# Kernel tuning notes

Hardware: AMD Instinct MI355X
Metric: run time of the kernel (lower is better)

The kernel has to match this reference:

```python
import jax, jax.numpy as jnp
import numpy as np


def setup_inputs() -> dict:
    key = jax.random.key(0)
    ks = jax.random.split(key, 9)
    B, Cin, H, W = 16, 512, 64, 64
    Cout = 256
    s_in = 0.02  # small init scale for stable softmax
    return {
        "x": jax.random.normal(ks[0], (B, Cin, H, W), dtype=jnp.float32),
        "Wq": jax.random.normal(ks[1], (Cout, Cin), dtype=jnp.float32) * s_in,
        "bq": jnp.zeros((Cout,), dtype=jnp.float32),
        "Wk": jax.random.normal(ks[2], (Cout, Cin), dtype=jnp.float32) * s_in,
        "bk": jnp.zeros((Cout,), dtype=jnp.float32),
        "Wv": jax.random.normal(ks[3], (Cout, Cin), dtype=jnp.float32) * s_in,
        "bv": jnp.zeros((Cout,), dtype=jnp.float32),
        "Wo": jax.random.normal(ks[4], (Cin, Cout), dtype=jnp.float32) * s_in,
        "bo": jnp.zeros((Cin,), dtype=jnp.float32),
    }


def reference(x, Wq, bq, Wk, bk, Wv, bv, Wo, bo):
    B, C, H, W = x.shape
    N = H * W
    xf = x.reshape(B, C, N)  # flatten spatial
    # 1x1 convs == per-pixel linear maps over channels
    q = jnp.einsum('oc,bcn->bon', Wq, xf) + bq[None, :, None]  # [B,Cout,N]
    k = jnp.einsum('oc,bcn->bon', Wk, xf) + bk[None, :, None]
    v = jnp.einsum('oc,bcn->bon', Wv, xf) + bv[None, :, None]
    # NOTE: original contracts over spatial dim N -> channel-attention [B,Cout,Cout]
    scale = jnp.asarray(N, x.dtype) ** 0.5  # query.size(-1) == N
    scores = jnp.einsum('bcn,bdn->bcd', q, k) / scale
    attn = jax.nn.softmax(scores, axis=-1)  # softmax over key-channel dim
    out = jnp.einsum('bcd,bdn->bcn', attn, v)  # [B,Cout,N]
    # permute(0,2,1).view(B,-1,H,W): row-major reshape of (B,N,Cout)
    out = jnp.transpose(out, (0, 2, 1)).reshape(B, -1, H, W)  # [B,Cout,H,W]
    out = jnp.einsum('co,bohw->bchw', Wo, out) + bo[None, :, None, None]
    return out
```

## Files before the change

kernel.cpp:

```cpp
#include <hip/hip_runtime.h>
#include <math.h>

typedef unsigned short u16;
typedef __bf16 bf16x8 __attribute__((ext_vector_type(8)));
typedef float f32x4 __attribute__((ext_vector_type(4)));
typedef unsigned short u16x4 __attribute__((ext_vector_type(4)));
typedef unsigned short u16x8 __attribute__((ext_vector_type(8)));

__device__ __forceinline__ u16 f2bf(float f) {
    unsigned int u = __float_as_uint(f);
    return (u16)((u + 0x7FFF + ((u >> 16) & 1)) >> 16);
}

#define BAR() do { __builtin_amdgcn_sched_barrier(0); __builtin_amdgcn_s_barrier(); __builtin_amdgcn_sched_barrier(0); } while (0)

__device__ __forceinline__ void stage_half(
    const u16* __restrict__ g, int ld, int row0, int rstride, int kt,
    u16* lds, int w, int l)
{
    #pragma unroll
    for (int qq = 0; qq < 2; ++qq) {
        const int c0 = qq * 512 + w * 64;
        const int c  = c0 + l;
        const int r  = c >> 3, kc = c & 7;
        const int kcg = kc ^ (r & 7);
        const u16* src = g + (size_t)(row0 + r * rstride) * ld + kt + kcg * 8;
        __builtin_amdgcn_global_load_lds(
            (const __attribute__((address_space(1))) unsigned int*)src,
            (__attribute__((address_space(3))) unsigned int*)(lds + (size_t)c0 * 8),
            16, 0, 0);
    }
}

#define QUAD(q_) do {                                                          \
    bf16x8 af0[2], af1[2];                                                     \
    { int row = wm + ((q_) * 2 + 0) * 16 + p;                                  \
      af0[0] = *(const bf16x8*)(bufA + row * 64 + ((0 + g) ^ (row & 7)) * 8);  \
      af0[1] = *(const bf16x8*)(bufA + row * 64 + ((4 + g) ^ (row & 7)) * 8); }\
    { int row = wm + ((q_) * 2 + 1) * 16 + p;                                  \
      af1[0] = *(const bf16x8*)(bufA + row * 64 + ((0 + g) ^ (row & 7)) * 8);  \
      af1[1] = *(const bf16x8*)(bufA + row * 64 + ((4 + g) ^ (row & 7)) * 8); }\
    __builtin_amdgcn_s_setprio(1);                                             \
    _Pragma("unroll")                                                          \
    for (int nf = 0; nf < 4; ++nf) {                                           \
        acc[(q_)*2+0][nf] = __builtin_amdgcn_mfma_f32_16x16x32_bf16(af0[0], bfr[nf][0], acc[(q_)*2+0][nf], 0, 0, 0); \
        acc[(q_)*2+0][nf] = __builtin_amdgcn_mfma_f32_16x16x32_bf16(af0[1], bfr[nf][1], acc[(q_)*2+0][nf], 0, 0, 0); \
        acc[(q_)*2+1][nf] = __builtin_amdgcn_mfma_f32_16x16x32_bf16(af1[0], bfr[nf][0], acc[(q_)*2+1][nf], 0, 0, 0); \
        acc[(q_)*2+1][nf] = __builtin_amdgcn_mfma_f32_16x16x32_bf16(af1[1], bfr[nf][1], acc[(q_)*2+1][nf], 0, 0, 0); \
    }                                                                          \
    __builtin_amdgcn_s_setprio(0);                                             \
} while (0)

template<int NT>
__device__ __forceinline__ void gemm256(
    const u16* __restrict__ Ag, int ldA, int baseA, int rsA,
    const u16* __restrict__ Bg, int ldB, int n0,
    u16* sm, f32x4 (&acc)[8][4])
{
    const int tid = threadIdx.x;
    const int l = tid & 63, w = tid >> 6;
    const int p = l & 15, g = l >> 4;
    const int wm = (w >> 2) * 128;
    const int wn = (w & 3) * 64;

    stage_half(Ag, ldA, baseA,             rsA, 0, sm,         w, l);
    stage_half(Ag, ldA, baseA + 128 * rsA, rsA, 0, sm + 8192,  w, l);
    stage_half(Bg, ldB, n0,       1, 0, sm + 16384, w, l);
    stage_half(Bg, ldB, n0 + 128, 1, 0, sm + 24576, w, l);

    for (int t = 0; t < NT; ++t) {
        u16* bufA  = sm + (t & 1) * 32768;
        u16* bufB  = bufA + 16384;
        u16* nbufA = sm + ((t + 1) & 1) * 32768;
        u16* nbufB = nbufA + 16384;
        const int kt1 = (t + 1) * 64;

        if (t + 1 < NT) {
            stage_half(Ag, ldA, baseA,             rsA, kt1, nbufA,        w, l);
            stage_half(Ag, ldA, baseA + 128 * rsA, rsA, kt1, nbufA + 8192, w, l);
            asm volatile("s_waitcnt vmcnt(4)" ::: "memory");
        } else {
            asm volatile("s_waitcnt vmcnt(0)" ::: "memory");
        }
        BAR();
        bf16x8 bfr[4][2];
        #pragma unroll
        for (int nf = 0; nf < 4; ++nf) {
            int row = wn + nf * 16 + p;
            bfr[nf][0] = *(const bf16x8*)(bufB + row * 64 + ((0 + g) ^ (row & 7)) * 8);
            bfr[nf][1] = *(const bf16x8*)(bufB + row * 64 + ((4 + g) ^ (row & 7)) * 8);
        }
        QUAD(0);
        BAR();
        if (t + 1 < NT) stage_half(Bg, ldB, n0, 1, kt1, nbufB, w, l);
        QUAD(1);
        BAR();
        if (t + 1 < NT) stage_half(Bg, ldB, n0 + 128, 1, kt1, nbufB + 8192, w, l);
        QUAD(2);
        BAR();
        QUAD(3);
        BAR();
    }
}

__device__ __forceinline__ void stage128(
    const u16* __restrict__ Ag, int ldA, const u16* __restrict__ Bg, int ldB,
    int m0, int n0, int k0, u16* Asm, u16* Bsm, int w, int l)
{
    const int row = (w & 1) * 64 + l;
    const int kbh = w >> 1;
    #pragma unroll
    for (int r = 0; r < 4; ++r) {
        const int kb = r * 2 + kbh;
        const u16* sa = Ag + (size_t)(m0 + row) * ldA + k0 + kb * 8;
        const u16* sb = Bg + (size_t)(n0 + row) * ldB + k0 + kb * 8;
        __builtin_amdgcn_global_load_lds(
            (const __attribute__((address_space(1))) unsigned int*)sa,
            (__attribute__((address_space(3))) unsigned int*)(Asm + (size_t)(r * 256 + w * 64) * 8),
            16, 0, 0);
        __builtin_amdgcn_global_load_lds(
            (const __attribute__((address_space(1))) unsigned int*)sb,
            (__attribute__((address_space(3))) unsigned int*)(Bsm + (size_t)(r * 256 + w * 64) * 8),
            16, 0, 0);
    }
}

__device__ __forceinline__ void compute128(
    const u16* Asm, const u16* Bsm, int wm, int wn, int p, int g, f32x4 acc[4][4])
{
    #pragma unroll
    for (int ks = 0; ks < 2; ++ks) {
        const int kb = ks * 4 + g;
        bf16x8 af[4], bfr[4];
        #pragma unroll
        for (int i = 0; i < 4; ++i)
            af[i] = *(const bf16x8*)(Asm + (size_t)(kb * 128 + wm + i * 16 + p) * 8);
        #pragma unroll
        for (int j = 0; j < 4; ++j)
            bfr[j] = *(const bf16x8*)(Bsm + (size_t)(kb * 128 + wn + j * 16 + p) * 8);
        #pragma unroll
        for (int i = 0; i < 4; ++i)
            #pragma unroll
            for (int j = 0; j < 4; ++j)
                acc[i][j] = __builtin_amdgcn_mfma_f32_16x16x32_bf16(af[i], bfr[j], acc[i][j], 0, 0, 0);
    }
}

__device__ __forceinline__ void gemm128(
    const u16* __restrict__ Ag, int ldA, const u16* __restrict__ Bg, int ldB,
    int m0, int n0, int kbeg, int ntiles, u16* Asm, u16* Bsm, f32x4 acc[4][4])
{
    const int tid = threadIdx.x;
    const int l = tid & 63, w = tid >> 6;
    const int p = l & 15, g = l >> 4;
    const int wm = (w >> 1) * 64, wn = (w & 1) * 64;

    stage128(Ag, ldA, Bg, ldB, m0, n0, kbeg, Asm, Bsm, w, l);
    for (int t = 0; t < ntiles; ++t) {
        __syncthreads();
        compute128(Asm, Bsm, wm, wn, p, g, acc);
        __syncthreads();
        if (t + 1 < ntiles)
            stage128(Ag, ldA, Bg, ldB, m0, n0, kbeg + (t + 1) * 64, Asm, Bsm, w, l);
    }
}

__global__ __launch_bounds__(256) void k0_xpose(const float* __restrict__ x, u16* __restrict__ xT)
{
    __shared__ float Tx[64 * 65];
    const int tid = threadIdx.x;
    const int b = blockIdx.z, c0 = blockIdx.y * 64, n0 = blockIdx.x * 64;
    const float* xb = x + (size_t)b * 512 * 4096;
    #pragma unroll
    for (int r = 0; r < 4; ++r) {
        int crow = (tid >> 4) + r * 16;
        int ncol = (tid & 15) * 4;
        float4 v = *(const float4*)(xb + (size_t)(c0 + crow) * 4096 + n0 + ncol);
        Tx[(ncol + 0) * 65 + crow] = v.x;
        Tx[(ncol + 1) * 65 + crow] = v.y;
        Tx[(ncol + 2) * 65 + crow] = v.z;
        Tx[(ncol + 3) * 65 + crow] = v.w;
    }
    __syncthreads();
    u16* ob = xT + (size_t)b * 4096 * 512;
    #pragma unroll
    for (int cc = 0; cc < 2; ++cc) {
        int id = cc * 256 + tid;
        int nrow = id >> 3;
        int cch = (id & 7) * 8;
        u16x8 u;
        #pragma unroll
        for (int j = 0; j < 8; ++j) u[j] = f2bf(Tx[nrow * 65 + cch + j]);
        *(u16x8*)(ob + (size_t)(n0 + nrow) * 512 + c0 + cch) = u;
    }
}

__global__ __launch_bounds__(256) void k0b_wconv(
    const float* __restrict__ s0, const float* __restrict__ s1,
    const float* __restrict__ s2, const float* __restrict__ s3,
    u16* __restrict__ d0, u16* __restrict__ d1, u16* __restrict__ d2, u16* __restrict__ d3)
{
    const int sel = blockIdx.y;
    const float* s = sel == 0 ? s0 : sel == 1 ? s1 : sel == 2 ? s2 : s3;
    u16* d = sel == 0 ? d0 : sel == 1 ? d1 : sel == 2 ? d2 : d3;
    int i = (blockIdx.x * 256 + threadIdx.x) * 4;
    float4 v = *(const float4*)(s + i);
    u16x4 u = {f2bf(v.x), f2bf(v.y), f2bf(v.z), f2bf(v.w)};
    *(u16x4*)(d + i) = u;
}

__global__ __launch_bounds__(512, 2) void k1a_qk(
    const u16* __restrict__ wqk, const float* __restrict__ bq, const float* __restrict__ bk,
    const u16* __restrict__ xT, u16* __restrict__ q, u16* __restrict__ kmat)
{
    __shared__ u16 sm[65536];
    const int b  = blockIdx.z;
    const int m0 = blockIdx.y * 256;
    const int n0 = blockIdx.x * 256;
    const u16* B = xT + (size_t)b * 4096 * 512;

    f32x4 acc[8][4] = {};
    gemm256<8>(wqk, 512, m0, 1, B, 512, n0, sm, acc);

    const int tid = threadIdx.x;
    const int l = tid & 63, w = tid >> 6;
    const int p = l & 15, g = l >> 4;
    const int wm = (w >> 2) * 128, wn = (w & 3) * 64;

    const float* bias = (m0 == 0) ? bq : bk;
    u16* outp = ((m0 == 0) ? q : kmat) + ((size_t)b << 20);
    #pragma unroll
    for (int mf = 0; mf < 8; ++mf)
        #pragma unroll
        for (int nf = 0; nf < 4; ++nf) {
            int n = n0 + wn + nf * 16 + p;
            #pragma unroll
            for (int r = 0; r < 4; ++r) {
                int mloc = wm + mf * 16 + g * 4 + r;
                outp[(size_t)mloc * 4096 + n] = f2bf(acc[mf][nf][r] + bias[mloc]);
            }
        }
}

__global__ __launch_bounds__(512, 2) void k1b_v(
    const u16* __restrict__ xT, const u16* __restrict__ wv, const float* __restrict__ bv,
    u16* __restrict__ vT)
{
    __shared__ u16 sm[65536];
    const int b  = blockIdx.z;
    const int m0 = blockIdx.x * 256;
    const u16* A = xT + (size_t)b * 4096 * 512;

    f32x4 acc[8][4] = {};
    gemm256<8>(A, 512, m0, 1, wv, 512, 0, sm, acc);

    const int tid = threadIdx.x;
    const int l = tid & 63, w = tid >> 6;
    const int p = l & 15, g = l >> 4;
    const int wm = (w >> 2) * 128, wn = (w & 3) * 64;

    u16* outp = vT + ((size_t)b << 20);
    #pragma unroll
    for (int nf = 0; nf < 4; ++nf) {
        int d = wn + nf * 16 + p;
        float bvv = bv[d];
        #pragma unroll
        for (int mf = 0; mf < 8; ++mf) {
            #pragma unroll
            for (int r = 0; r < 4; ++r) {
                int row = m0 + wm + mf * 16 + g * 4 + r;
                outp[(size_t)row * 256 + d] = f2bf(acc[mf][nf][r] + bvv);
            }
        }
    }
}

__global__ __launch_bounds__(256) void k2_scores(
    const u16* __restrict__ q, const u16* __restrict__ kmat, float* __restrict__ spart)
{
    __shared__ u16 sm[16384];
    const int bz = blockIdx.z;
    const int b = bz >> 3, split = bz & 7;
    const int m0 = blockIdx.y * 128, n0 = blockIdx.x * 128;
    const u16* A = q    + ((size_t)b << 20);
    const u16* B = kmat + ((size_t)b << 20);

    f32x4 acc[4][4] = {};
    gemm128(A, 4096, B, 4096, m0, n0, split * 512, 8, sm, sm + 8192, acc);

    const int tid = threadIdx.x;
    const int l = tid & 63, w = tid >> 6;
    const int p = l & 15, g = l >> 4;
    const int wm = (w >> 1) * 64, wn = (w & 1) * 64;
    float* sp = spart + ((size_t)split * 16 + b) * 65536;
    #pragma unroll
    for (int mf = 0; mf < 4; ++mf)
        #pragma unroll
        for (int nf = 0; nf < 4; ++nf) {
            int n = n0 + wn + nf * 16 + p;
            #pragma unroll
            for (int r = 0; r < 4; ++r) {
                int m = m0 + wm + mf * 16 + g * 4 + r;
                sp[(size_t)m * 256 + n] = acc[mf][nf][r] * 0.015625f;
            }
        }
}

__global__ __launch_bounds__(256) void k3_softmax(
    const float* __restrict__ sp, u16* __restrict__ attn)
{
    const int row = blockIdx.x;
    const int tid = threadIdx.x;
    const size_t STRIDE = (size_t)16 * 65536;
    const size_t base = (size_t)row * 256 + tid;

    float s = 0.f;
    #pragma unroll
    for (int i = 0; i < 8; ++i) s += sp[base + i * STRIDE];

    __shared__ float red[4];
    float m = s;
    #pragma unroll
    for (int off = 32; off >= 1; off >>= 1) m = fmaxf(m, __shfl_xor(m, off));
    if ((tid & 63) == 0) red[tid >> 6] = m;
    __syncthreads();
    m = fmaxf(fmaxf(red[0], red[1]), fmaxf(red[2], red[3]));

    float e = expf(s - m);
    float t = e;
    #pragma unroll
    for (int off = 32; off >= 1; off >>= 1) t += __shfl_xor(t, off);
    __syncthreads();
    if ((tid & 63) == 0) red[tid >> 6] = t;
    __syncthreads();
    t = red[0] + red[1] + red[2] + red[3];

    attn[base] = f2bf(e / t);
}

__global__ __launch_bounds__(512, 2) void k4_pv(
    const u16* __restrict__ attn, const u16* __restrict__ vT, u16* __restrict__ outT3)
{
    __shared__ u16 sm[65536];
    const int b  = blockIdx.z;
    const int sh = blockIdx.x;
    const u16* A = vT   + ((size_t)b << 20);
    const u16* B = attn + ((size_t)b << 16);

    f32x4 acc[8][4] = {};
    gemm256<4>(A, 256, sh, 16, B, 256, 0, sm, acc);

    const int tid = threadIdx.x;
    const int l = tid & 63, w = tid >> 6;
    const int p = l & 15, g = l >> 4;
    const int wm = (w >> 2) * 128, wn = (w & 3) * 64;

    u16* outp = outT3 + (((size_t)b * 16 + sh) << 16);
    #pragma unroll
    for (int mf = 0; mf < 8; ++mf)
        #pragma unroll
        for (int nf = 0; nf < 4; ++nf) {
            int co  = wn + nf * 16 + p;
            int nh0 = wm + mf * 16 + g * 4;
            u16x4 u = {f2bf(acc[mf][nf][0]), f2bf(acc[mf][nf][1]),
                       f2bf(acc[mf][nf][2]), f2bf(acc[mf][nf][3])};
            *(u16x4*)(outp + (size_t)co * 256 + nh0) = u;
        }
}

__global__ __launch_bounds__(512, 2) void k5_final(
    const u16* __restrict__ wo, const float* __restrict__ bo,
    const u16* __restrict__ outT3, float* __restrict__ out)
{
    __shared__ u16 sm[65536];
    const int bz = blockIdx.z;
    const int b  = bz >> 4, sh = bz & 15;
    const int m0 = blockIdx.y * 256;
    const u16* B = outT3 + ((size_t)bz << 16);

    f32x4 acc[8][4] = {};
    gemm256<4>(wo, 256, m0, 1, B, 256, 0, sm, acc);

    const int tid = threadIdx.x;
    const int l = tid & 63, w = tid >> 6;
    const int p = l & 15, g = l >> 4;
    const int wm = (w >> 2) * 128, wn = (w & 3) * 64;

    float* ob = out + (size_t)b * 2097152 + (size_t)sh * 256;
    #pragma unroll
    for (int mf = 0; mf < 8; ++mf)
        #pragma unroll
        for (int nf = 0; nf < 4; ++nf) {
            int slo = wn + nf * 16 + p;
            #pragma unroll
            for (int r = 0; r < 4; ++r) {
                int m = m0 + wm + mf * 16 + g * 4 + r;
                ob[(size_t)m * 4096 + slo] = acc[mf][nf][r] + bo[m];
            }
        }
}

extern "C" void kernel_launch(void* const* d_in, const int* in_sizes, int n_in,
                              void* d_out, int out_size, void* d_ws, size_t ws_size,
                              hipStream_t stream) {
    (void)in_sizes; (void)n_in; (void)out_size; (void)ws_size;
    const float* x  = (const float*)d_in[0];
    const float* Wq = (const float*)d_in[1];
    const float* bq = (const float*)d_in[2];
    const float* Wk = (const float*)d_in[3];
    const float* bk = (const float*)d_in[4];
    const float* Wv = (const float*)d_in[5];
    const float* bv = (const float*)d_in[6];
    const float* Wo = (const float*)d_in[7];
    const float* bo = (const float*)d_in[8];
    float* out = (float*)d_out;

    char* ws = (char*)d_ws;
    u16* xT   = (u16*)(ws + 0);
    u16* q    = (u16*)(ws + 67108864);
    u16* kmat = (u16*)(ws + 100663296);
    u16* vT   = (u16*)(ws + 134217728);
    float* spart = (float*)(ws + 0);
    u16* attn    = (u16*)(ws + 67108864);
    u16* outT3   = (u16*)(ws + 100663296);
    u16* wqk  = (u16*)(ws + 167772160);
    u16* wv   = (u16*)(ws + 168296448);
    u16* wo   = (u16*)(ws + 168558592);

    k0b_wconv <<<dim3(128, 4),    dim3(256), 0, stream>>>(Wq, Wk, Wv, Wo,
                                                          wqk, wqk + 131072, wv, wo);
    k0_xpose  <<<dim3(64, 8, 16), dim3(256), 0, stream>>>(x, xT);
    k1a_qk    <<<dim3(16, 2, 16), dim3(512), 0, stream>>>(wqk, bq, bk, xT, q, kmat);
    k1b_v     <<<dim3(16, 1, 16), dim3(512), 0, stream>>>(xT, wv, bv, vT);
    k2_scores <<<dim3(2, 2, 128), dim3(256), 0, stream>>>(q, kmat, spart);
    k3_softmax<<<dim3(4096),      dim3(256), 0, stream>>>(spart, attn);
    k4_pv     <<<dim3(16, 1, 16), dim3(512), 0, stream>>>(attn, vT, outT3);
    k5_final  <<<dim3(1, 2, 256), dim3(512), 0, stream>>>(wo, bo, outT3, out);
}
```

Measured before the change: 220.1 us.

## Merge prep and QKV launches, retile scores GEMM with 16-way K split

Weight conversion is folded into the transpose kernel as an extra z-slice, and the QK and V projection kernels become one launch that branches on blockIdx.y. This removes two kernel launches and lets the projection work share one grid. The scores GEMM moves from 128x128 tiles with an 8-way K split to full 256x256 tiles with a 16-way split over gemm256. Softmax now sums 16 partial score buffers, which doubles the partial-sum traffic through the fp32 spart workspace in exchange for fewer, larger GEMM blocks.

```diff
diff --git a/kernel.cpp b/kernel.cpp
--- a/kernel.cpp
+++ b/kernel.cpp
@@ -103,72 +103,26 @@
     }
 }
 
-__device__ __forceinline__ void stage128(
-    const u16* __restrict__ Ag, int ldA, const u16* __restrict__ Bg, int ldB,
-    int m0, int n0, int k0, u16* Asm, u16* Bsm, int w, int l)
-{
-    const int row = (w & 1) * 64 + l;
-    const int kbh = w >> 1;
-    #pragma unroll
-    for (int r = 0; r < 4; ++r) {
-        const int kb = r * 2 + kbh;
-        const u16* sa = Ag + (size_t)(m0 + row) * ldA + k0 + kb * 8;
-        const u16* sb = Bg + (size_t)(n0 + row) * ldB + k0 + kb * 8;
-        __builtin_amdgcn_global_load_lds(
-            (const __attribute__((address_space(1))) unsigned int*)sa,
-            (__attribute__((address_space(3))) unsigned int*)(Asm + (size_t)(r * 256 + w * 64) * 8),
-            16, 0, 0);
-        __builtin_amdgcn_global_load_lds(
-            (const __attribute__((address_space(1))) unsigned int*)sb,
-            (__attribute__((address_space(3))) unsigned int*)(Bsm + (size_t)(r * 256 + w * 64) * 8),
-            16, 0, 0);
-    }
-}
-
-__device__ __forceinline__ void compute128(
-    const u16* Asm, const u16* Bsm, int wm, int wn, int p, int g, f32x4 acc[4][4])
-{
-    #pragma unroll
-    for (int ks = 0; ks < 2; ++ks) {
-        const int kb = ks * 4 + g;
-        bf16x8 af[4], bfr[4];
-        #pragma unroll
-        for (int i = 0; i < 4; ++i)
-            af[i] = *(const bf16x8*)(Asm + (size_t)(kb * 128 + wm + i * 16 + p) * 8);
-        #pragma unroll
-        for (int j = 0; j < 4; ++j)
-            bfr[j] = *(const bf16x8*)(Bsm + (size_t)(kb * 128 + wn + j * 16 + p) * 8);
-        #pragma unroll
-        for (int i = 0; i < 4; ++i)
-            #pragma unroll
-            for (int j = 0; j < 4; ++j)
-                acc[i][j] = __builtin_amdgcn_mfma_f32_16x16x32_bf16(af[i], bfr[j], acc[i][j], 0, 0, 0);
-    }
-}
-
-__device__ __forceinline__ void gemm128(
-    const u16* __restrict__ Ag, int ldA, const u16* __restrict__ Bg, int ldB,
-    int m0, int n0, int kbeg, int ntiles, u16* Asm, u16* Bsm, f32x4 acc[4][4])
-{
-    const int tid = threadIdx.x;
-    const int l = tid & 63, w = tid >> 6;
-    const int p = l & 15, g = l >> 4;
-    const int wm = (w >> 1) * 64, wn = (w & 1) * 64;
-
-    stage128(Ag, ldA, Bg, ldB, m0, n0, kbeg, Asm, Bsm, w, l);
-    for (int t = 0; t < ntiles; ++t) {
-        __syncthreads();
-        compute128(Asm, Bsm, wm, wn, p, g, acc);
-        __syncthreads();
-        if (t + 1 < ntiles)
-            stage128(Ag, ldA, Bg, ldB, m0, n0, kbeg + (t + 1) * 64, Asm, Bsm, w, l);
-    }
-}
-
-__global__ __launch_bounds__(256) void k0_xpose(const float* __restrict__ x, u16* __restrict__ xT)
-{
+__global__ __launch_bounds__(256) void k0_prep(
+    const float* __restrict__ x, u16* __restrict__ xT,
+    const float* __restrict__ Wq, const float* __restrict__ Wk,
+    const float* __restrict__ Wv, const float* __restrict__ Wo,
+    u16* __restrict__ wqk, u16* __restrict__ wv, u16* __restrict__ wo)
+{
+    const int tid = threadIdx.x;
+    if (blockIdx.z == 16) {
+        const int bid = blockIdx.y * 64 + blockIdx.x;
+        const int sel = bid >> 7;
+        const int sub = bid & 127;
+        const float* s = sel == 0 ? Wq : sel == 1 ? Wk : sel == 2 ? Wv : Wo;
+        u16* d = sel == 0 ? wqk : sel == 1 ? (wqk + 131072) : sel == 2 ? wv : wo;
+        int i = (sub * 256 + tid) * 4;
+        float4 v = *(const float4*)(s + i);
+        u16x4 u = {f2bf(v.x), f2bf(v.y), f2bf(v.z), f2bf(v.w)};
+        *(u16x4*)(d + i) = u;
+        return;
+    }
     __shared__ float Tx[64 * 65];
-    const int tid = threadIdx.x;
     const int b = blockIdx.z, c0 = blockIdx.y * 64, n0 = blockIdx.x * 64;
     const float* xb = x + (size_t)b * 512 * 4096;
     #pragma unroll
@@ -195,112 +149,89 @@
     }
 }
 
-__global__ __launch_bounds__(256) void k0b_wconv(
-    const float* __restrict__ s0, const float* __restrict__ s1,
-    const float* __restrict__ s2, const float* __restrict__ s3,
-    u16* __restrict__ d0, u16* __restrict__ d1, u16* __restrict__ d2, u16* __restrict__ d3)
-{
-    const int sel = blockIdx.y;
-    const float* s = sel == 0 ? s0 : sel == 1 ? s1 : sel == 2 ? s2 : s3;
-    u16* d = sel == 0 ? d0 : sel == 1 ? d1 : sel == 2 ? d2 : d3;
-    int i = (blockIdx.x * 256 + threadIdx.x) * 4;
-    float4 v = *(const float4*)(s + i);
-    u16x4 u = {f2bf(v.x), f2bf(v.y), f2bf(v.z), f2bf(v.w)};
-    *(u16x4*)(d + i) = u;
-}
-
-__global__ __launch_bounds__(512, 2) void k1a_qk(
-    const u16* __restrict__ wqk, const float* __restrict__ bq, const float* __restrict__ bk,
-    const u16* __restrict__ xT, u16* __restrict__ q, u16* __restrict__ kmat)
+__global__ __launch_bounds__(512, 2) void k1_qkv(
+    const u16* __restrict__ wqk, const u16* __restrict__ wv,
+    const float* __restrict__ bq, const float* __restrict__ bk, const float* __restrict__ bv,
+    const u16* __restrict__ xT, u16* __restrict__ q, u16* __restrict__ kmat,
+    u16* __restrict__ vT)
 {
     __shared__ u16 sm[65536];
-    const int b  = blockIdx.z;
-    const int m0 = blockIdx.y * 256;
-    const int n0 = blockIdx.x * 256;
-    const u16* B = xT + (size_t)b * 4096 * 512;
+    const int b = blockIdx.z;
+    const int y = blockIdx.y;
+    const u16* xb = xT + (size_t)b * 4096 * 512;
+
+    const int tid = threadIdx.x;
+    const int l = tid & 63, w = tid >> 6;
+    const int p = l & 15, g = l >> 4;
+    const int wm = (w >> 2) * 128, wn = (w & 3) * 64;
 
     f32x4 acc[8][4] = {};
-    gemm256<8>(wqk, 512, m0, 1, B, 512, n0, sm, acc);
+
+    if (y < 2) {
+        const int m0 = y * 256;
+        const int n0 = blockIdx.x * 256;
+        gemm256<8>(wqk, 512, m0, 1, xb, 512, n0, sm, acc);
+
+        const float* bias = (y == 0) ? bq : bk;
+        u16* outp = ((y == 0) ? q : kmat) + ((size_t)b << 20);
+        #pragma unroll
+        for (int mf = 0; mf < 8; ++mf)
+            #pragma unroll
+            for (int nf = 0; nf < 4; ++nf) {
+                int n = n0 + wn + nf * 16 + p;
+                #pragma unroll
+                for (int r = 0; r < 4; ++r) {
+                    int mloc = wm + mf * 16 + g * 4 + r;
+                    outp[(size_t)mloc * 4096 + n] = f2bf(acc[mf][nf][r] + bias[mloc]);
+                }
+            }
+    } else {
+        const int m0 = blockIdx.x * 256;
+        gemm256<8>(xb, 512, m0, 1, wv, 512, 0, sm, acc);
+
+        u16* outp = vT + ((size_t)b << 20);
+        #pragma unroll
+        for (int nf = 0; nf < 4; ++nf) {
+            int d = wn + nf * 16 + p;
+            float bvv = bv[d];
+            #pragma unroll
+            for (int mf = 0; mf < 8; ++mf) {
+                #pragma unroll
+                for (int r = 0; r < 4; ++r) {
+                    int row = m0 + wm + mf * 16 + g * 4 + r;
+                    outp[(size_t)row * 256 + d] = f2bf(acc[mf][nf][r] + bvv);
+                }
+            }
+        }
+    }
+}
+
+__global__ __launch_bounds__(512, 2) void k2_scores(
+    const u16* __restrict__ q, const u16* __restrict__ kmat, float* __restrict__ spart)
+{
+    __shared__ u16 sm[65536];
+    const int b = blockIdx.z;
+    const int split = blockIdx.x;
+    const u16* A = q    + ((size_t)b << 20) + split * 256;
+    const u16* B = kmat + ((size_t)b << 20) + split * 256;
+
+    f32x4 acc[8][4] = {};
+    gemm256<4>(A, 4096, 0, 1, B, 4096, 0, sm, acc);
 
     const int tid = threadIdx.x;
     const int l = tid & 63, w = tid >> 6;
     const int p = l & 15, g = l >> 4;
     const int wm = (w >> 2) * 128, wn = (w & 3) * 64;
 
-    const float* bias = (m0 == 0) ? bq : bk;
-    u16* outp = ((m0 == 0) ? q : kmat) + ((size_t)b << 20);
+    float* sp = spart + ((size_t)split * 16 + b) * 65536;
     #pragma unroll
     for (int mf = 0; mf < 8; ++mf)
         #pragma unroll
         for (int nf = 0; nf < 4; ++nf) {
-            int n = n0 + wn + nf * 16 + p;
+            int n = wn + nf * 16 + p;
             #pragma unroll
             for (int r = 0; r < 4; ++r) {
-                int mloc = wm + mf * 16 + g * 4 + r;
-                outp[(size_t)mloc * 4096 + n] = f2bf(acc[mf][nf][r] + bias[mloc]);
-            }
-        }
-}
-
-__global__ __launch_bounds__(512, 2) void k1b_v(
-    const u16* __restrict__ xT, const u16* __restrict__ wv, const float* __restrict__ bv,
-    u16* __restrict__ vT)
-{
-    __shared__ u16 sm[65536];
-    const int b  = blockIdx.z;
-    const int m0 = blockIdx.x * 256;
-    const u16* A = xT + (size_t)b * 4096 * 512;
-
-    f32x4 acc[8][4] = {};
-    gemm256<8>(A, 512, m0, 1, wv, 512, 0, sm, acc);
-
-    const int tid = threadIdx.x;
-    const int l = tid & 63, w = tid >> 6;
-    const int p = l & 15, g = l >> 4;
-    const int wm = (w >> 2) * 128, wn = (w & 3) * 64;
-
-    u16* outp = vT + ((size_t)b << 20);
-    #pragma unroll
-    for (int nf = 0; nf < 4; ++nf) {
-        int d = wn + nf * 16 + p;
-        float bvv = bv[d];
-        #pragma unroll
-        for (int mf = 0; mf < 8; ++mf) {
-            #pragma unroll
-            for (int r = 0; r < 4; ++r) {
-                int row = m0 + wm + mf * 16 + g * 4 + r;
-                outp[(size_t)row * 256 + d] = f2bf(acc[mf][nf][r] + bvv);
-            }
-        }
-    }
-}
-
-__global__ __launch_bounds__(256) void k2_scores(
-    const u16* __restrict__ q, const u16* __restrict__ kmat, float* __restrict__ spart)
-{
-    __shared__ u16 sm[16384];
-    const int bz = blockIdx.z;
-    const int b = bz >> 3, split = bz & 7;
-    const int m0 = blockIdx.y * 128, n0 = blockIdx.x * 128;
-    const u16* A = q    + ((size_t)b << 20);
-    const u16* B = kmat + ((size_t)b << 20);
-
-    f32x4 acc[4][4] = {};
-    gemm128(A, 4096, B, 4096, m0, n0, split * 512, 8, sm, sm + 8192, acc);
-
-    const int tid = threadIdx.x;
-    const int l = tid & 63, w = tid >> 6;
-    const int p = l & 15, g = l >> 4;
-    const int wm = (w >> 1) * 64, wn = (w & 1) * 64;
-    float* sp = spart + ((size_t)split * 16 + b) * 65536;
-    #pragma unroll
-    for (int mf = 0; mf < 4; ++mf)
-        #pragma unroll
-        for (int nf = 0; nf < 4; ++nf) {
-            int n = n0 + wn + nf * 16 + p;
-            #pragma unroll
-            for (int r = 0; r < 4; ++r) {
-                int m = m0 + wm + mf * 16 + g * 4 + r;
+                int m = wm + mf * 16 + g * 4 + r;
                 sp[(size_t)m * 256 + n] = acc[mf][nf][r] * 0.015625f;
             }
         }
@@ -316,7 +247,7 @@
 
     float s = 0.f;
     #pragma unroll
-    for (int i = 0; i < 8; ++i) s += sp[base + i * STRIDE];
+    for (int i = 0; i < 16; ++i) s += sp[base + i * STRIDE];
 
     __shared__ float red[4];
     float m = s;
@@ -427,12 +358,9 @@
     u16* wv   = (u16*)(ws + 168296448);
     u16* wo   = (u16*)(ws + 168558592);
 
-    k0b_wconv <<<dim3(128, 4),    dim3(256), 0, stream>>>(Wq, Wk, Wv, Wo,
-                                                          wqk, wqk + 131072, wv, wo);
-    k0_xpose  <<<dim3(64, 8, 16), dim3(256), 0, stream>>>(x, xT);
-    k1a_qk    <<<dim3(16, 2, 16), dim3(512), 0, stream>>>(wqk, bq, bk, xT, q, kmat);
-    k1b_v     <<<dim3(16, 1, 16), dim3(512), 0, stream>>>(xT, wv, bv, vT);
-    k2_scores <<<dim3(2, 2, 128), dim3(256), 0, stream>>>(q, kmat, spart);
+    k0_prep   <<<dim3(64, 8, 17), dim3(256), 0, stream>>>(x, xT, Wq, Wk, Wv, Wo, wqk, wv, wo);
+    k1_qkv    <<<dim3(16, 3, 16), dim3(512), 0, stream>>>(wqk, wv, bq, bk, bv, xT, q, kmat, vT);
+    k2_scores <<<dim3(16, 1, 16), dim3(512), 0, stream>>>(q, kmat, spart);
     k3_softmax<<<dim3(4096),      dim3(256), 0, stream>>>(spart, attn);
     k4_pv     <<<dim3(16, 1, 16), dim3(512), 0, stream>>>(attn, vT, outT3);
     k5_final  <<<dim3(1, 2, 256), dim3(512), 0, stream>>>(wo, bo, outT3, out);
```

New measurement: 200.4 us. 1.1x faster.
